# Kernel optimization log

Hardware: AMD Instinct MI355X
Metric: run time of the kernel (lower is better)

## Reference

```python
import jax, jax.numpy as jnp
import numpy as np

D_MODEL = 2048
NUM_HEADS = 16
NUM_KV_HEADS = 4
HEAD_DIM = D_MODEL // NUM_HEADS  # 128
ROPE_THETA = 10000.0
BATCH = 2
SEQ = 2048


def _rotate_half(x):
    # interleaved rotate-half: pairs (x0,x1) -> (-x1, x0)
    x1 = x[..., ::2]
    x2 = x[..., 1::2]
    return jnp.stack((-x2, x1), axis=-1).reshape(x.shape)


def _rope_tables(seq_len, dtype, start_pos=0):
    inv_freq = 1.0 / (ROPE_THETA ** (jnp.arange(0, HEAD_DIM, 2, dtype=jnp.float32) / HEAD_DIM))
    positions = jnp.arange(start_pos, start_pos + seq_len, dtype=jnp.float32)
    freqs = jnp.outer(positions, inv_freq)              # [S, HD/2]
    emb = jnp.repeat(freqs, 2, axis=-1)                  # [S, HD]
    cos = jnp.cos(emb).astype(dtype)[None, None, :, :]   # [1,1,S,HD]
    sin = jnp.sin(emb).astype(dtype)[None, None, :, :]
    return cos, sin


def setup_inputs() -> dict:
    key = jax.random.key(0)
    ks = jax.random.split(key, 5)
    s = 0.02
    x = jax.random.normal(ks[0], (BATCH, SEQ, D_MODEL), dtype=jnp.float32)
    wq = jax.random.normal(ks[1], (D_MODEL, NUM_HEADS * HEAD_DIM), dtype=jnp.float32) * s
    wk = jax.random.normal(ks[2], (D_MODEL, NUM_KV_HEADS * HEAD_DIM), dtype=jnp.float32) * s
    wv = jax.random.normal(ks[3], (D_MODEL, NUM_KV_HEADS * HEAD_DIM), dtype=jnp.float32) * s
    wo = jax.random.normal(ks[4], (D_MODEL, D_MODEL), dtype=jnp.float32) * s
    return {"x": x, "wq": wq, "wk": wk, "wv": wv, "wo": wo}


def reference(x, wq, wk, wv, wo):
    batch, seq_len, _ = x.shape
    # projections (bias-free linears)
    q = (x @ wq).reshape(batch, seq_len, NUM_HEADS, HEAD_DIM).transpose(0, 2, 1, 3)
    k = (x @ wk).reshape(batch, seq_len, NUM_KV_HEADS, HEAD_DIM).transpose(0, 2, 1, 3)
    v = (x @ wv).reshape(batch, seq_len, NUM_KV_HEADS, HEAD_DIM).transpose(0, 2, 1, 3)
    # RoPE
    cos, sin = _rope_tables(seq_len, q.dtype)
    q = q * cos + _rotate_half(q) * sin
    k = k * cos + _rotate_half(k) * sin
    # GQA: duplicate KV heads
    repeats = NUM_HEADS // NUM_KV_HEADS
    k = jnp.repeat(k, repeats, axis=1)
    v = jnp.repeat(v, repeats, axis=1)
    # causal SDPA
    scale = HEAD_DIM ** -0.5
    scores = jnp.einsum('bhqd,bhkd->bhqk', q, k) * scale
    causal = jnp.tril(jnp.ones((seq_len, seq_len), dtype=bool))
    scores = jnp.where(causal[None, None, :, :], scores, -jnp.inf)
    weights = jax.nn.softmax(scores, axis=-1)
    y = jnp.einsum('bhqk,bhkd->bhqd', weights, v)
    y = y.transpose(0, 2, 1, 3).reshape(batch, seq_len, NUM_HEADS * HEAD_DIM)
    return y @ wo
```

## Files before the change

kernel.cpp:

```cpp
#include <hip/hip_runtime.h>
#include <cstdint>
#include <cstddef>

using short8 = __attribute__((ext_vector_type(8))) short;
using f32x4  = __attribute__((ext_vector_type(4))) float;
using u16x4  = __attribute__((ext_vector_type(4))) unsigned short;

#define DEV __device__ __forceinline__

DEV unsigned short f2bf(float f) {
  unsigned int u = __builtin_bit_cast(unsigned int, f);
  u += 0x7fffu + ((u >> 16) & 1u);
  return (unsigned short)(u >> 16);
}
DEV float bf2f(unsigned short h) {
  unsigned int u = ((unsigned int)h) << 16;
  return __builtin_bit_cast(float, u);
}
DEV unsigned int cvtpk_bf16(float lo, float hi) {
  unsigned int d;
  asm("v_cvt_pk_bf16_f32 %0, %1, %2" : "=v"(d) : "v"(lo), "v"(hi));
  return d;
}

#define GLL16(gp, lp)                                                          \
  __builtin_amdgcn_global_load_lds(                                            \
      (const __attribute__((address_space(1))) char*)(const char*)(gp),        \
      (__attribute__((address_space(3))) char*)(char*)(lp), 16, 0, 0)

constexpr int BATCH = 2, SEQ = 2048, DMODEL = 2048, NH = 16, NKVH = 4, DH = 128;
constexpr int MROWS = BATCH * SEQ;
constexpr int NQKV  = DMODEL + 2 * NKVH * DH;
constexpr int KOFF  = DMODEL;
constexpr int VOFF  = DMODEL + NKVH * DH;
constexpr float SM_L2 = 0.12751388158f;


__global__ void k_tables(float* __restrict__ tc, float* __restrict__ ts) {
  int id = blockIdx.x * 256 + threadIdx.x;
  int pos = id >> 6, i = id & 63;
  float freq = __expf(-(float)i * 0.14391157f);
  float ang = (float)pos * freq;
  tc[id] = cosf(ang);
  ts[id] = sinf(ang);
}

__global__ void k_castx(const float* __restrict__ x, unsigned short* __restrict__ xb) {
  int id = blockIdx.x * 256 + threadIdx.x;
  float4 v = ((const float4*)x)[id];
  u16x4 o = { f2bf(v.x), f2bf(v.y), f2bf(v.z), f2bf(v.w) };
  ((u16x4*)xb)[id] = o;
}

__global__ __launch_bounds__(256) void k_wtrans(const float* __restrict__ src,
                                                unsigned short* __restrict__ dst, int N) {
  __shared__ float tile[32][33];
  int n0 = blockIdx.x * 32, k0 = blockIdx.y * 32;
  int tx = threadIdx.x, ty = threadIdx.y;
  #pragma unroll
  for (int r = ty; r < 32; r += 8)
    tile[r][tx] = src[(size_t)(k0 + r) * N + n0 + tx];
  __syncthreads();
  #pragma unroll
  for (int r = ty; r < 32; r += 8)
    dst[(size_t)(n0 + r) * 2048 + k0 + tx] = f2bf(tile[tx][r]);
}

__global__ __launch_bounds__(256) void k_vtrans(const unsigned short* __restrict__ qkv,
                                                unsigned short* __restrict__ vt) {
  __shared__ unsigned short tile[32][33];
  int s0 = blockIdx.x * 32, d0 = blockIdx.y * 32;
  int bk = blockIdx.z;
  const unsigned short* src = qkv + (size_t)(bk >> 2) * SEQ * NQKV + VOFF + (bk & 3) * DH;
  unsigned short* dst = vt + ((size_t)bk * DH + d0) * SEQ + s0;
  int tx = threadIdx.x, ty = threadIdx.y;
  #pragma unroll
  for (int r = ty; r < 32; r += 8)
    tile[r][tx] = src[(size_t)(s0 + r) * NQKV + d0 + tx];
  __syncthreads();
  #pragma unroll
  for (int r = ty; r < 32; r += 8)
    dst[(size_t)r * SEQ + tx] = tile[tx][r];
}


template <int BNT, bool OUTF32, bool ROPE>
__global__ __launch_bounds__(512, 2) void k_gemm256(
    const unsigned short* __restrict__ A,
    const unsigned short* __restrict__ Bt,
    void* __restrict__ C, int M, int N, int K,
    const float* __restrict__ tc, const float* __restrict__ ts) {
  constexpr int NF = BNT / 64;
  __shared__ unsigned short As[2][256 * 64];
  __shared__ unsigned short Bs[2][BNT * 64];

  const int t = threadIdx.x, l = t & 63, w = t >> 6;
  const int rl = l & 15, kg = l >> 4;
  const int wm = w >> 2, wn = w & 3;

  const int gx = gridDim.x;
  const int nwg = gx * gridDim.y;
  const int idl = blockIdx.y * gx + blockIdx.x;
  const int swz = (idl & 7) * (nwg >> 3) + (idl >> 3);
  const int m0 = (swz / gx) * 256, n0 = (swz % gx) * BNT;

  const unsigned short* aSrc[4];
  const unsigned short* bSrc[NF];
  #pragma unroll
  for (int i = 0; i < 4; ++i) {
    int c = i * 512 + t, row = c >> 3, q = c & 7;
    aSrc[i] = A + (size_t)(m0 + row) * K + ((q ^ (row & 7)) << 3);
  }
  #pragma unroll
  for (int i = 0; i < NF; ++i) {
    int c = i * 512 + t, row = c >> 3, q = c & 7;
    bSrc[i] = Bt + (size_t)(n0 + row) * K + ((q ^ (row & 7)) << 3);
  }

  f32x4 acc[8][NF] = {};

  const int nk = K / 64;
  #pragma unroll
  for (int i = 0; i < 4; ++i) GLL16(aSrc[i], (char*)As[0] + i * 8192 + t * 16);
  #pragma unroll
  for (int i = 0; i < NF; ++i) GLL16(bSrc[i], (char*)Bs[0] + i * 8192 + t * 16);

  int cur = 0;
  for (int kt = 0; kt < nk; ++kt) {
    if (kt + 1 < nk) {
      const int off = (kt + 1) * 64;
      #pragma unroll
      for (int i = 0; i < 4; ++i)
        GLL16(aSrc[i] + off, (char*)As[cur ^ 1] + i * 8192 + t * 16);
      #pragma unroll
      for (int i = 0; i < NF; ++i)
        GLL16(bSrc[i] + off, (char*)Bs[cur ^ 1] + i * 8192 + t * 16);
      if constexpr (NF == 4)      asm volatile("s_waitcnt vmcnt(8)" ::: "memory");
      else if constexpr (NF == 3) asm volatile("s_waitcnt vmcnt(7)" ::: "memory");
      else                        asm volatile("s_waitcnt vmcnt(6)" ::: "memory");
    } else {
      asm volatile("s_waitcnt vmcnt(0)" ::: "memory");
    }
    __builtin_amdgcn_sched_barrier(0);
    __builtin_amdgcn_s_barrier();

    const unsigned short* a = As[cur];
    const unsigned short* b = Bs[cur];
    auto rdA = [&](int mf, int ks) {
      int row = wm * 128 + mf * 16 + rl;
      return *(const short8*)&a[row * 64 + (((ks * 4 + kg) ^ (row & 7)) << 3)];
    };
    auto rdB = [&](int nf, int ks) {
      int row = wn * (BNT / 4) + nf * 16 + rl;
      return *(const short8*)&b[row * 64 + (((ks * 4 + kg) ^ (row & 7)) << 3)];
    };

    short8 aF[4][2], bF[NF][2];
    #pragma unroll
    for (int mi = 0; mi < 4; ++mi)
      #pragma unroll
      for (int ks = 0; ks < 2; ++ks) aF[mi][ks] = rdA(mi, ks);
    #pragma unroll
    for (int j = 0; j < NF; ++j) {
      #pragma unroll
      for (int ks = 0; ks < 2; ++ks) bF[j][ks] = rdB(j, ks);
      __builtin_amdgcn_s_setprio(1);
      #pragma unroll
      for (int mi = 0; mi < 4; ++mi)
        #pragma unroll
        for (int ks = 0; ks < 2; ++ks)
          acc[mi][j] = __builtin_amdgcn_mfma_f32_16x16x32_bf16(aF[mi][ks], bF[j][ks], acc[mi][j], 0, 0, 0);
      __builtin_amdgcn_s_setprio(0);
    }
    #pragma unroll
    for (int mi = 0; mi < 4; ++mi)
      #pragma unroll
      for (int ks = 0; ks < 2; ++ks) aF[mi][ks] = rdA(4 + mi, ks);
    #pragma unroll
    for (int j = 0; j < NF; ++j) {
      __builtin_amdgcn_s_setprio(1);
      #pragma unroll
      for (int mi = 0; mi < 4; ++mi)
        #pragma unroll
        for (int ks = 0; ks < 2; ++ks)
          acc[4 + mi][j] = __builtin_amdgcn_mfma_f32_16x16x32_bf16(aF[mi][ks], bF[j][ks], acc[4 + mi][j], 0, 0, 0);
      __builtin_amdgcn_s_setprio(0);
    }

    __builtin_amdgcn_s_barrier();
    cur ^= 1;
  }

  #pragma unroll
  for (int mf = 0; mf < 8; ++mf) {
    #pragma unroll
    for (int nf = 0; nf < NF; ++nf) {
      const int row0 = m0 + wm * 128 + mf * 16 + kg * 4;
      const int colb = n0 + wn * (BNT / 4) + nf * 16;
      const int col = colb + rl;
      if constexpr (ROPE) {
        if (colb < VOFF) {
          const int dd = (col & 127) >> 1;
          const float sgn = (col & 1) ? 1.0f : -1.0f;
          const float qs = (colb < KOFF) ? SM_L2 : 1.0f;
          #pragma unroll
          for (int r = 0; r < 4; ++r) {
            const int s = (row0 + r) & (SEQ - 1);
            const float c = tc[s * 64 + dd], sn = ts[s * 64 + dd];
            const float xv = acc[mf][nf][r];
            const float xp = __shfl_xor(xv, 1);
            acc[mf][nf][r] = (xv * c + sgn * xp * sn) * qs;
          }
        }
      }
      #pragma unroll
      for (int r = 0; r < 4; ++r) {
        if constexpr (OUTF32)
          ((float*)C)[(size_t)(row0 + r) * N + col] = acc[mf][nf][r];
        else
          ((unsigned short*)C)[(size_t)(row0 + r) * N + col] = f2bf(acc[mf][nf][r]);
      }
    }
  }
}


constexpr int QB = 128, KB = 64;
constexpr float THR = 8.0f;

__global__ __launch_bounds__(512, 4) void k_attn(const unsigned short* __restrict__ qkv,
                                                 const unsigned short* __restrict__ vt,
                                                 unsigned short* __restrict__ obuf) {
  __shared__ unsigned short Ks[2][KB * DH];
  __shared__ unsigned short Vs[2][DH * KB];
  __shared__ unsigned short Pw[8][16 * 64];

  const int t = threadIdx.x, l = t & 63, w = t >> 6;
  const int rl = l & 15, kg = l >> 4;

  const int id = blockIdx.x;
  const int b = id >> 8;
  const int u = id & 255;
  const int h = u >> 4;
  const int qtr = u & 15;
  const int qt = b ? (15 - qtr) : qtr;
  const int q0 = qt * QB;
  const int kvh = h >> 2;

  const unsigned short* qbase = qkv + (size_t)b * SEQ * NQKV;
  const unsigned short* kbase = qbase + KOFF + kvh * DH;
  const unsigned short* vtb = vt + (size_t)(b * NKVH + kvh) * DH * SEQ;

  const unsigned short* kp[2];
  const unsigned short* vp[2];
  #pragma unroll
  for (int i = 0; i < 2; ++i) {
    int c = i * 512 + t;
    int krow = c >> 4, kq = c & 15;
    kp[i] = kbase + (size_t)krow * NQKV + ((kq ^ (krow & 7)) << 3);
    int vrow = c >> 3, vq = c & 7;
    vp[i] = vtb + (size_t)vrow * SEQ + ((vq ^ (vrow & 7)) << 3);
  }

  const int qw0 = q0 + w * 16;

  short8 qF[4];
  {
    const size_t qr = (size_t)(qw0 + rl) * NQKV + h * DH;
    #pragma unroll
    for (int ks = 0; ks < 4; ++ks)
      qF[ks] = *(const short8*)(qbase + qr + ks * 32 + kg * 8);
  }

  f32x4 Oc[8] = {};
  float mr = -3e38f, lr = 0.f;

  char* pwB = (char*)Pw[w] + rl * 128;
  const int pkey = (rl & 7) << 4;
  const int nt = q0 / KB + 2;

  #pragma unroll
  for (int i = 0; i < 2; ++i) {
    GLL16(kp[i], (char*)Ks[0] + w * 1024 + i * 8192);
    GLL16(vp[i], (char*)Vs[0] + w * 1024 + i * 8192);
  }

  int cur = 0;
  for (int tt = 0; tt < nt; ++tt) {
    const int kv0 = tt * KB;
    const bool more = (tt + 1 < nt);
    if (more) {
      #pragma unroll
      for (int i = 0; i < 2; ++i) {
        GLL16(kp[i] + (size_t)(kv0 + KB) * NQKV, (char*)Ks[cur ^ 1] + w * 1024 + i * 8192);
        GLL16(vp[i] + (kv0 + KB),               (char*)Vs[cur ^ 1] + w * 1024 + i * 8192);
      }
      asm volatile("s_waitcnt vmcnt(4)" ::: "memory");
    } else {
      asm volatile("s_waitcnt vmcnt(0)" ::: "memory");
    }
    __builtin_amdgcn_sched_barrier(0);
    __builtin_amdgcn_s_barrier();

    if (kv0 < qw0 + 16) {
      const unsigned short* KsC = Ks[cur];
      const unsigned short* VsC = Vs[cur];

      f32x4 St[4] = {};
      __builtin_amdgcn_s_setprio(1);
      #pragma unroll
      for (int n = 0; n < 4; ++n) {
        const int kr = n * 16 + rl;
        #pragma unroll
        for (int ks = 0; ks < 4; ++ks) {
          short8 kF = *(const short8*)&KsC[kr * DH + (((ks * 4 + kg) ^ (kr & 7)) << 3)];
          St[n] = __builtin_amdgcn_mfma_f32_16x16x32_bf16(kF, qF[ks], St[n], 0, 0, 0);
        }
      }
      __builtin_amdgcn_s_setprio(0);

      float mx = -3e38f;
      const bool diag = (kv0 + KB - 1) > qw0;
      if (diag) {
        const int thr = qw0 + rl - kv0;
        #pragma unroll
        for (int n = 0; n < 4; ++n)
          #pragma unroll
          for (int r = 0; r < 4; ++r) {
            float s = St[n][r];
            if (n * 16 + kg * 4 + r > thr) s = -3e38f;
            St[n][r] = s;
            mx = fmaxf(mx, s);
          }
      } else {
        #pragma unroll
        for (int n = 0; n < 4; ++n)
          #pragma unroll
          for (int r = 0; r < 4; ++r) mx = fmaxf(mx, St[n][r]);
      }
      mx = fmaxf(mx, __shfl_xor(mx, 16));
      mx = fmaxf(mx, __shfl_xor(mx, 32));

      if (__any(mx > mr + THR)) {
        const float mnew = fmaxf(mr, mx);
        const float sf = exp2f(mr - mnew);
        mr = mnew;
        lr *= sf;
        float sfv[4];
        #pragma unroll
        for (int r = 0; r < 4; ++r) sfv[r] = __shfl(sf, kg * 4 + r, 16);
        #pragma unroll
        for (int c = 0; c < 8; ++c)
          #pragma unroll
          for (int r = 0; r < 4; ++r) Oc[c][r] *= sfv[r];
      }

      float rs = 0.f;
      #pragma unroll
      for (int n = 0; n < 4; ++n) {
        float e0 = exp2f(St[n][0] - mr);
        float e1 = exp2f(St[n][1] - mr);
        float e2 = exp2f(St[n][2] - mr);
        float e3 = exp2f(St[n][3] - mr);
        rs += (e0 + e1) + (e2 + e3);
        uint2 d;
        d.x = cvtpk_bf16(e0, e1);
        d.y = cvtpk_bf16(e2, e3);
        *(uint2*)(pwB + ((n * 32 + kg * 8) ^ pkey)) = d;
      }
      rs += __shfl_xor(rs, 16);
      rs += __shfl_xor(rs, 32);
      lr += rs;

      short8 pF[2];
      #pragma unroll
      for (int ks2 = 0; ks2 < 2; ++ks2)
        pF[ks2] = *(const short8*)(pwB + ((ks2 * 64 + kg * 16) ^ pkey));
      __builtin_amdgcn_s_setprio(1);
      #pragma unroll
      for (int c = 0; c < 8; ++c) {
        const int vr = c * 16 + rl;
        #pragma unroll
        for (int ks2 = 0; ks2 < 2; ++ks2) {
          short8 vF = *(const short8*)&VsC[vr * KB + (((ks2 * 4 + kg) ^ (vr & 7)) << 3)];
          Oc[c] = __builtin_amdgcn_mfma_f32_16x16x32_bf16(pF[ks2], vF, Oc[c], 0, 0, 0);
        }
      }
      __builtin_amdgcn_s_setprio(0);
    }

    __builtin_amdgcn_s_barrier();
    cur ^= 1;
  }

  const float linv = 1.0f / lr;
  float inv[4];
  #pragma unroll
  for (int r = 0; r < 4; ++r) inv[r] = __shfl(linv, kg * 4 + r, 16);
  #pragma unroll
  for (int c = 0; c < 8; ++c)
    #pragma unroll
    for (int r = 0; r < 4; ++r) {
      int row = b * SEQ + qw0 + kg * 4 + r;
      obuf[(size_t)row * DMODEL + h * DH + c * 16 + rl] = f2bf(Oc[c][r] * inv[r]);
    }
}


extern "C" void kernel_launch(void* const* d_in, const int* in_sizes, int n_in,
                              void* d_out, int out_size, void* d_ws, size_t ws_size,
                              hipStream_t stream) {
  const float* x  = (const float*)d_in[0];
  const float* wq = (const float*)d_in[1];
  const float* wk = (const float*)d_in[2];
  const float* wv = (const float*)d_in[3];
  const float* wo = (const float*)d_in[4];
  float* out = (float*)d_out;

  unsigned short* xb  = (unsigned short*)d_ws;
  unsigned short* wT  = xb  + (size_t)MROWS * DMODEL;
  unsigned short* woT = wT  + (size_t)NQKV * DMODEL;
  unsigned short* qkv = woT + (size_t)DMODEL * DMODEL;
  unsigned short* ob  = qkv + (size_t)MROWS * NQKV;
  float* tc = (float*)(ob + (size_t)MROWS * DMODEL);
  float* ts = tc + SEQ * 64;
  unsigned short* vtG = wT;

  k_tables<<<dim3(SEQ * 64 / 256), dim3(256), 0, stream>>>(tc, ts);
  k_castx<<<dim3(MROWS * DMODEL / 4 / 256), dim3(256), 0, stream>>>(x, xb);
  k_wtrans<<<dim3(DMODEL / 32, 64), dim3(32, 8), 0, stream>>>(wq, wT, DMODEL);
  k_wtrans<<<dim3(NKVH * DH / 32, 64), dim3(32, 8), 0, stream>>>(wk, wT + (size_t)DMODEL * 2048, NKVH * DH);
  k_wtrans<<<dim3(NKVH * DH / 32, 64), dim3(32, 8), 0, stream>>>(wv, wT + (size_t)VOFF * 2048, NKVH * DH);
  k_wtrans<<<dim3(DMODEL / 32, 64), dim3(32, 8), 0, stream>>>(wo, woT, DMODEL);

  k_gemm256<192, false, true><<<dim3(NQKV / 192, MROWS / 256), dim3(512), 0, stream>>>(
      xb, wT, qkv, MROWS, NQKV, DMODEL, tc, ts);
  k_vtrans<<<dim3(SEQ / 32, DH / 32, BATCH * NKVH), dim3(32, 8), 0, stream>>>(qkv, vtG);
  k_attn<<<dim3(512), dim3(512), 0, stream>>>(qkv, vtG, ob);
  k_gemm256<128, true, false><<<dim3(DMODEL / 128, MROWS / 256), dim3(512), 0, stream>>>(
      ob, woT, out, MROWS, DMODEL, DMODEL, nullptr, nullptr);
}
```

Before: 220.1 us.

## Interleave GEMM global prefetch with MFMA phases and merge weight transposes

```diff
diff --git a/kernel.cpp b/kernel.cpp
--- a/kernel.cpp
+++ b/kernel.cpp
@@ -52,10 +52,19 @@
   ((u16x4*)xb)[id] = o;
 }
 
-__global__ __launch_bounds__(256) void k_wtrans(const float* __restrict__ src,
-                                                unsigned short* __restrict__ dst, int N) {
+__global__ __launch_bounds__(256) void k_wtrans4(
+    const float* __restrict__ wq, const float* __restrict__ wk,
+    const float* __restrict__ wv, const float* __restrict__ wo,
+    unsigned short* __restrict__ wT, unsigned short* __restrict__ woT) {
   __shared__ float tile[32][33];
+  const int z = blockIdx.z;
+  const float* src; unsigned short* dst; int N;
+  if (z == 0)      { src = wq; dst = wT;                        N = 2048; }
+  else if (z == 1) { src = wo; dst = woT;                       N = 2048; }
+  else if (z == 2) { src = wk; dst = wT + (size_t)KOFF * 2048;  N = 512; }
+  else             { src = wv; dst = wT + (size_t)VOFF * 2048;  N = 512; }
   int n0 = blockIdx.x * 32, k0 = blockIdx.y * 32;
+  if (n0 >= N) return;
   int tx = threadIdx.x, ty = threadIdx.y;
   #pragma unroll
   for (int r = ty; r < 32; r += 8)
@@ -90,7 +99,8 @@
     const unsigned short* __restrict__ Bt,
     void* __restrict__ C, int M, int N, int K,
     const float* __restrict__ tc, const float* __restrict__ ts) {
-  constexpr int NF = BNT / 64;
+  constexpr int NF  = BNT / 64;
+  constexpr int NFA = (NF + 1) / 2;
   __shared__ unsigned short As[2][256 * 64];
   __shared__ unsigned short Bs[2][BNT * 64];
 
@@ -124,28 +134,17 @@
   for (int i = 0; i < 4; ++i) GLL16(aSrc[i], (char*)As[0] + i * 8192 + t * 16);
   #pragma unroll
   for (int i = 0; i < NF; ++i) GLL16(bSrc[i], (char*)Bs[0] + i * 8192 + t * 16);
+  asm volatile("s_waitcnt vmcnt(0)" ::: "memory");
+  __builtin_amdgcn_s_barrier();
 
   int cur = 0;
   for (int kt = 0; kt < nk; ++kt) {
-    if (kt + 1 < nk) {
-      const int off = (kt + 1) * 64;
-      #pragma unroll
-      for (int i = 0; i < 4; ++i)
-        GLL16(aSrc[i] + off, (char*)As[cur ^ 1] + i * 8192 + t * 16);
-      #pragma unroll
-      for (int i = 0; i < NF; ++i)
-        GLL16(bSrc[i] + off, (char*)Bs[cur ^ 1] + i * 8192 + t * 16);
-      if constexpr (NF == 4)      asm volatile("s_waitcnt vmcnt(8)" ::: "memory");
-      else if constexpr (NF == 3) asm volatile("s_waitcnt vmcnt(7)" ::: "memory");
-      else                        asm volatile("s_waitcnt vmcnt(6)" ::: "memory");
-    } else {
-      asm volatile("s_waitcnt vmcnt(0)" ::: "memory");
-    }
-    __builtin_amdgcn_sched_barrier(0);
-    __builtin_amdgcn_s_barrier();
-
+    const bool more = kt + 1 < nk;
+    const int off = (kt + 1) * 64;
     const unsigned short* a = As[cur];
     const unsigned short* b = Bs[cur];
+    char* An = (char*)As[cur ^ 1];
+    char* Bn = (char*)Bs[cur ^ 1];
     auto rdA = [&](int mf, int ks) {
       int row = wm * 128 + mf * 16 + rl;
       return *(const short8*)&a[row * 64 + (((ks * 4 + kg) ^ (row & 7)) << 3)];
@@ -154,40 +153,87 @@
       int row = wn * (BNT / 4) + nf * 16 + rl;
       return *(const short8*)&b[row * 64 + (((ks * 4 + kg) ^ (row & 7)) << 3)];
     };
-
     short8 aF[4][2], bF[NF][2];
+
     #pragma unroll
     for (int mi = 0; mi < 4; ++mi)
       #pragma unroll
       for (int ks = 0; ks < 2; ++ks) aF[mi][ks] = rdA(mi, ks);
     #pragma unroll
-    for (int j = 0; j < NF; ++j) {
+    for (int j = 0; j < NFA; ++j)
       #pragma unroll
       for (int ks = 0; ks < 2; ++ks) bF[j][ks] = rdB(j, ks);
-      __builtin_amdgcn_s_setprio(1);
-      #pragma unroll
-      for (int mi = 0; mi < 4; ++mi)
+    if (more) {
+      GLL16(aSrc[0] + off, An + 0 * 8192 + t * 16);
+      GLL16(aSrc[1] + off, An + 1 * 8192 + t * 16);
+    }
+    __builtin_amdgcn_s_barrier();
+    __builtin_amdgcn_s_setprio(1);
+    #pragma unroll
+    for (int mi = 0; mi < 4; ++mi)
+      #pragma unroll
+      for (int j = 0; j < NFA; ++j)
         #pragma unroll
         for (int ks = 0; ks < 2; ++ks)
           acc[mi][j] = __builtin_amdgcn_mfma_f32_16x16x32_bf16(aF[mi][ks], bF[j][ks], acc[mi][j], 0, 0, 0);
-      __builtin_amdgcn_s_setprio(0);
-    }
+    __builtin_amdgcn_s_setprio(0);
+    __builtin_amdgcn_s_barrier();
+
+    #pragma unroll
+    for (int j = NFA; j < NF; ++j)
+      #pragma unroll
+      for (int ks = 0; ks < 2; ++ks) bF[j][ks] = rdB(j, ks);
+    if (more) {
+      GLL16(aSrc[2] + off, An + 2 * 8192 + t * 16);
+      GLL16(aSrc[3] + off, An + 3 * 8192 + t * 16);
+    }
+    __builtin_amdgcn_s_barrier();
+    __builtin_amdgcn_s_setprio(1);
+    #pragma unroll
+    for (int mi = 0; mi < 4; ++mi)
+      #pragma unroll
+      for (int j = NFA; j < NF; ++j)
+        #pragma unroll
+        for (int ks = 0; ks < 2; ++ks)
+          acc[mi][j] = __builtin_amdgcn_mfma_f32_16x16x32_bf16(aF[mi][ks], bF[j][ks], acc[mi][j], 0, 0, 0);
+    __builtin_amdgcn_s_setprio(0);
+    __builtin_amdgcn_s_barrier();
+
     #pragma unroll
     for (int mi = 0; mi < 4; ++mi)
       #pragma unroll
       for (int ks = 0; ks < 2; ++ks) aF[mi][ks] = rdA(4 + mi, ks);
-    #pragma unroll
-    for (int j = 0; j < NF; ++j) {
-      __builtin_amdgcn_s_setprio(1);
-      #pragma unroll
-      for (int mi = 0; mi < 4; ++mi)
+    if (more) {
+      #pragma unroll
+      for (int i = 0; i < NF; ++i)
+        GLL16(bSrc[i] + off, Bn + i * 8192 + t * 16);
+    }
+    __builtin_amdgcn_s_barrier();
+    __builtin_amdgcn_s_setprio(1);
+    #pragma unroll
+    for (int mi = 0; mi < 4; ++mi)
+      #pragma unroll
+      for (int j = 0; j < NFA; ++j)
         #pragma unroll
         for (int ks = 0; ks < 2; ++ks)
           acc[4 + mi][j] = __builtin_amdgcn_mfma_f32_16x16x32_bf16(aF[mi][ks], bF[j][ks], acc[4 + mi][j], 0, 0, 0);
-      __builtin_amdgcn_s_setprio(0);
-    }
-
-    __builtin_amdgcn_s_barrier();
+    __builtin_amdgcn_s_setprio(0);
+    __builtin_amdgcn_s_barrier();
+
+    asm volatile("s_waitcnt vmcnt(0)" ::: "memory");
+    __builtin_amdgcn_sched_barrier(0);
+    __builtin_amdgcn_s_barrier();
+    __builtin_amdgcn_s_setprio(1);
+    #pragma unroll
+    for (int mi = 0; mi < 4; ++mi)
+      #pragma unroll
+      for (int j = NFA; j < NF; ++j)
+        #pragma unroll
+        for (int ks = 0; ks < 2; ++ks)
+          acc[4 + mi][j] = __builtin_amdgcn_mfma_f32_16x16x32_bf16(aF[mi][ks], bF[j][ks], acc[4 + mi][j], 0, 0, 0);
+    __builtin_amdgcn_s_setprio(0);
+    __builtin_amdgcn_s_barrier();
+
     cur ^= 1;
   }
 
@@ -428,10 +474,7 @@
 
   k_tables<<<dim3(SEQ * 64 / 256), dim3(256), 0, stream>>>(tc, ts);
   k_castx<<<dim3(MROWS * DMODEL / 4 / 256), dim3(256), 0, stream>>>(x, xb);
-  k_wtrans<<<dim3(DMODEL / 32, 64), dim3(32, 8), 0, stream>>>(wq, wT, DMODEL);
-  k_wtrans<<<dim3(NKVH * DH / 32, 64), dim3(32, 8), 0, stream>>>(wk, wT + (size_t)DMODEL * 2048, NKVH * DH);
-  k_wtrans<<<dim3(NKVH * DH / 32, 64), dim3(32, 8), 0, stream>>>(wv, wT + (size_t)VOFF * 2048, NKVH * DH);
-  k_wtrans<<<dim3(DMODEL / 32, 64), dim3(32, 8), 0, stream>>>(wo, woT, DMODEL);
+  k_wtrans4<<<dim3(64, 64, 4), dim3(32, 8), 0, stream>>>(wq, wk, wv, wo, wT, woT);
 
   k_gemm256<192, false, true><<<dim3(NQKV / 192, MROWS / 256), dim3(512), 0, stream>>>(
       xb, wT, qkv, MROWS, NQKV, DMODEL, tc, ts);
```

New measurement: 221.9 us. About the same (+0.8%).
